# Kernel optimization log

Hardware: AMD Instinct MI355X
Metric: run time of the kernel (lower is better)

Reference implementation:

```python
import jax, jax.numpy as jnp
import numpy as np


def apply_rope(x):
    # x: [B, T, H, D]
    T, D = x.shape[1], x.shape[3]
    inv_freq = 1.0 / (10000.0 ** (jnp.arange(0, D, 2, dtype=jnp.float32) / D))  # [D/2]
    t = jnp.arange(T, dtype=jnp.float32)
    freqs = jnp.outer(t, inv_freq)  # [T, D/2]
    sin_f = jnp.sin(freqs)[None, :, None, :]
    cos_f = jnp.cos(freqs)[None, :, None, :]
    x1, x2 = jnp.split(x, 2, axis=-1)
    return jnp.concatenate([x1 * cos_f - x2 * sin_f, x1 * sin_f + x2 * cos_f], axis=-1)


def setup_inputs() -> dict:
    key = jax.random.key(0)
    ks = jax.random.split(key, 5)
    B, T, D = 8, 8192, 128
    s = 1.0 / np.sqrt(D)
    return {
        "x": jax.random.normal(ks[0], (B, T, D), dtype=jnp.float32),
        "Wq": jax.random.normal(ks[1], (D, D), dtype=jnp.float32) * s,
        "bq": jnp.zeros((D,), dtype=jnp.float32),
        "Wk": jax.random.normal(ks[2], (D, D), dtype=jnp.float32) * s,
        "bk": jnp.zeros((D,), dtype=jnp.float32),
        "Wv": jax.random.normal(ks[3], (D, D), dtype=jnp.float32) * s,
        "bv": jnp.zeros((D,), dtype=jnp.float32),
        "Wo": jax.random.normal(ks[4], (D, D), dtype=jnp.float32) * s,
        "bo": jnp.zeros((D,), dtype=jnp.float32),
    }


def reference(x, Wq, bq, Wk, bk, Wv, bv, Wo, bo):
    n_heads = 8
    B, T, d_model = x.shape
    head_dim = d_model // n_heads

    q = (x @ Wq + bq).reshape(B, T, n_heads, head_dim)
    k = (x @ Wk + bk).reshape(B, T, n_heads, head_dim)
    v = (x @ Wv + bv).reshape(B, T, n_heads, head_dim)

    q = jax.nn.elu(apply_rope(q)) + 1.0
    k = jax.nn.elu(apply_rope(k)) + 1.0

    # non-causal linear attention: context = sum_t k_t v_t^T per head
    context = jnp.einsum("bthd,bthe->bhde", k, v)            # [B,H,Dh,Dh]
    out = jnp.einsum("bthd,bhde->bthe", q, context)           # [B,T,H,Dh]
    k_sum = jnp.sum(k, axis=1)                                  # [B,H,Dh]
    z = 1.0 / (jnp.einsum("bthd,bhd->bth", q, k_sum) + 1e-6)  # [B,T,H]
    out = out * z[..., None]

    out = out.reshape(B, T, d_model)
    return out @ Wo + bo
```

## Files before the change

kernel.cpp:

```cpp
#include <hip/hip_runtime.h>
#include <hip/hip_bf16.h>


typedef __attribute__((ext_vector_type(8))) short short8;
typedef __attribute__((ext_vector_type(4))) float floatx4;

#define DEV __device__ __forceinline__
#define MFMA __builtin_amdgcn_mfma_f32_16x16x32_bf16

DEV unsigned short bfh(float f) {
  unsigned int x = __float_as_uint(f);
  x += 0x7fffu + ((x >> 16) & 1u);
  return (unsigned short)(x >> 16);
}
DEV float bfdec(unsigned short u) { return __uint_as_float(((unsigned int)u) << 16); }
DEV void splitf(float f, unsigned short& h, unsigned short& l) {
  h = bfh(f);
  l = bfh(f - bfdec(h));
}
DEV void split8(const float* p, short8& h8, short8& l8) {
  float4 a = *(const float4*)p;
  float4 b = *(const float4*)(p + 4);
  float v[8] = {a.x, a.y, a.z, a.w, b.x, b.y, b.z, b.w};
  union { short8 s; unsigned short u[8]; } H, L;
#pragma unroll
  for (int i = 0; i < 8; ++i) splitf(v[i], H.u[i], L.u[i]);
  h8 = H.s; l8 = L.s;
}

DEV void xpose_frag(floatx4 m0, floatx4 m1, int lane16, int quad,
                    short8& hi, short8& lo) {
  union { short8 s; unsigned short u[8]; } H, L;
#pragma unroll
  for (int j = 0; j < 8; ++j) {
    int srcLane = lane16 + (((quad & 1) * 2 + (j >> 2)) << 4);
    float vA = __shfl(m0[j & 3], srcLane, 64);
    float vB = __shfl(m1[j & 3], srcLane, 64);
    float v = (quad < 2) ? vA : vB;
    splitf(v, H.u[j], L.u[j]);
  }
  hi = H.s; lo = L.s;
}

__global__ void k_prep(const float* __restrict__ Wq, const float* __restrict__ Wk,
                       const float* __restrict__ Wv,
                       unsigned short* __restrict__ WTh, unsigned short* __restrict__ WTl,
                       float* __restrict__ ctxz) {
  int gid = blockIdx.x * 256 + threadIdx.x;
  if (gid < 6144) {
    int mat = gid >> 11, r = gid & 2047, n = r >> 4, k0 = (r & 15) * 8;
    const float* W = (mat == 0) ? Wq : (mat == 1) ? Wk : Wv;
    union { uint4 q; unsigned short u[8]; } oh, ol;
#pragma unroll
    for (int i = 0; i < 8; ++i) splitf(W[(size_t)(k0 + i) * 128 + n], oh.u[i], ol.u[i]);
    *(uint4*)&WTh[mat * 16384 + n * 128 + k0] = oh.q;
    *(uint4*)&WTl[mat * 16384 + n * 128 + k0] = ol.q;
  } else if (gid < 6144 + 17408) {
    ctxz[gid - 6144] = 0.0f;
  }
}

__global__ __launch_bounds__(512) void k_qkv(
    const float* __restrict__ x,
    const unsigned short* __restrict__ WTh, const unsigned short* __restrict__ WTl,
    const float* __restrict__ bq, const float* __restrict__ bk, const float* __restrict__ bv,
    float* __restrict__ ctx, float* __restrict__ ksum,
    unsigned short* __restrict__ qws) {
  __shared__ unsigned short xh[64 * 136], xl[64 * 136];
  __shared__ float rc[64][9], rs[64][9];
  const int tid = threadIdx.x;
  const int row0 = blockIdx.x * 64;
  const int b = row0 >> 13;
  const int t0 = row0 & 8191;

  {
    int r = tid >> 3, j = tid & 7;
    float invf = 1.0f / powf(10000.0f, (float)j * 0.125f);
    float s, c;
    sincosf((float)(t0 + r) * invf, &s, &c);
    rc[r][j] = c; rs[r][j] = s;
  }
  {
    int r = tid >> 3, cg = (tid & 7) * 16;
    const float* xp = x + (size_t)(row0 + r) * 128 + cg;
    short8 h0, l0, h1, l1;
    split8(xp, h0, l0);
    split8(xp + 8, h1, l1);
    *(short8*)&xh[r * 136 + cg] = h0;
    *(short8*)&xh[r * 136 + cg + 8] = h1;
    *(short8*)&xl[r * 136 + cg] = l0;
    *(short8*)&xl[r * 136 + cg + 8] = l1;
  }
  __syncthreads();

  const int l = tid & 63, w = tid >> 6;
  const int lane16 = l & 15, quad = l >> 4;

  floatx4 acc[3][4];
#pragma unroll
  for (int i = 0; i < 3; ++i)
#pragma unroll
    for (int j = 0; j < 4; ++j) acc[i][j] = (floatx4){0.f, 0.f, 0.f, 0.f};

#pragma unroll
  for (int ks = 0; ks < 4; ++ks) {
    short8 afh[4], afl[4];
#pragma unroll
    for (int mt = 0; mt < 4; ++mt) {
      int off = (mt * 16 + lane16) * 136 + ks * 32 + quad * 8;
      afh[mt] = *(const short8*)&xh[off];
      afl[mt] = *(const short8*)&xl[off];
    }
#pragma unroll
    for (int mat = 0; mat < 3; ++mat) {
      size_t woff = (size_t)mat * 16384 +
                    (size_t)(w * 16 + lane16) * 128 + ks * 32 + quad * 8;
      short8 bh = *(const short8*)(WTh + woff);
      short8 bl = *(const short8*)(WTl + woff);
#pragma unroll
      for (int mt = 0; mt < 4; ++mt) {
        acc[mat][mt] = MFMA(afh[mt], bh, acc[mat][mt], 0, 0, 0);
        acc[mat][mt] = MFMA(afl[mt], bh, acc[mat][mt], 0, 0, 0);
        acc[mat][mt] = MFMA(afh[mt], bl, acc[mat][mt], 0, 0, 0);
      }
    }
  }

  {
    int col = w * 16 + lane16;
    float bias[3] = {bq[col], bk[col], bv[col]};
#pragma unroll
    for (int mat = 0; mat < 3; ++mat)
#pragma unroll
      for (int mt = 0; mt < 4; ++mt)
#pragma unroll
        for (int r = 0; r < 4; ++r) acc[mat][mt][r] += bias[mat];
  }

  {
    const int d = lane16, j = d & 7;
#pragma unroll
    for (int mt = 0; mt < 4; ++mt) {
      float cc[4], ss[4];
#pragma unroll
      for (int r = 0; r < 4; ++r) {
        int tl = mt * 16 + quad * 4 + r;
        cc[r] = rc[tl][j]; ss[r] = rs[tl][j];
      }
#pragma unroll
      for (int mat = 0; mat < 2; ++mat) {
#pragma unroll
        for (int r = 0; r < 4; ++r) {
          float v = acc[mat][mt][r];
          float p = __shfl_xor(v, 8);
          float nv = (d < 8) ? (v * cc[r] - p * ss[r]) : (p * ss[r] + v * cc[r]);
          acc[mat][mt][r] = (nv > 0.f) ? (nv + 1.f) : __expf(nv);
        }
      }
    }
  }

  {
    float s = 0.f;
#pragma unroll
    for (int mt = 0; mt < 4; ++mt)
#pragma unroll
      for (int r = 0; r < 4; ++r) s += acc[1][mt][r];
    s += __shfl_xor(s, 16);
    s += __shfl_xor(s, 32);
    if (l < 16) atomicAdd(&ksum[(b * 8 + w) * 16 + lane16], s);
  }

#pragma unroll
  for (int mt = 0; mt < 4; ++mt)
#pragma unroll
    for (int r = 0; r < 4; ++r)
      qws[(size_t)(row0 + mt * 16 + quad * 4 + r) * 128 + w * 16 + lane16] =
          bfh(acc[0][mt][r]);

  {
    floatx4 c = (floatx4){0.f, 0.f, 0.f, 0.f};
#pragma unroll
    for (int ks2 = 0; ks2 < 2; ++ks2) {
      short8 kh, kl, vh, vl;
      xpose_frag(acc[1][ks2 * 2], acc[1][ks2 * 2 + 1], lane16, quad, kh, kl);
      xpose_frag(acc[2][ks2 * 2], acc[2][ks2 * 2 + 1], lane16, quad, vh, vl);
      c = MFMA(kh, vh, c, 0, 0, 0);
      c = MFMA(kl, vh, c, 0, 0, 0);
      c = MFMA(kh, vl, c, 0, 0, 0);
    }
#pragma unroll
    for (int r = 0; r < 4; ++r)
      atomicAdd(&ctx[((size_t)(b * 8 + w) * 16 + quad * 4 + r) * 16 + lane16], c[r]);
  }
}

__global__ void k_mprep(const float* __restrict__ Wo, const float* __restrict__ ctx,
                        unsigned short* __restrict__ MTh, unsigned short* __restrict__ MTl) {
  int gid = blockIdx.x * 256 + threadIdx.x;
  int b = gid >> 11, r = gid & 2047, oc = r >> 4, qcg = r & 15;
  int h = qcg >> 1, d0 = (qcg & 1) * 8;
  const float* C = ctx + (size_t)(b * 8 + h) * 256;
  float m[8] = {0.f, 0.f, 0.f, 0.f, 0.f, 0.f, 0.f, 0.f};
#pragma unroll 4
  for (int e = 0; e < 16; ++e) {
    float wv = Wo[(size_t)(h * 16 + e) * 128 + oc];
#pragma unroll
    for (int i = 0; i < 8; ++i) m[i] += C[(d0 + i) * 16 + e] * wv;
  }
  union { uint4 q; unsigned short u[8]; } oh, ol;
#pragma unroll
  for (int i = 0; i < 8; ++i) splitf(m[i], oh.u[i], ol.u[i]);
  *(uint4*)&MTh[(size_t)gid * 8] = oh.q;
  *(uint4*)&MTl[(size_t)gid * 8] = ol.q;
}

__global__ __launch_bounds__(256) void k_zout(
    const unsigned short* __restrict__ qws,
    const unsigned short* __restrict__ MTh, const unsigned short* __restrict__ MTl,
    const float* __restrict__ bo, const float* __restrict__ ksum,
    float* __restrict__ out) {
  __shared__ float ksumS[128], boS[128];
  const int tid = threadIdx.x;
  const int row0 = blockIdx.x * 128;
  const int b = row0 >> 13;

  if (tid < 128) ksumS[tid] = ksum[b * 128 + tid];
  else boS[tid - 128] = bo[tid - 128];
  __syncthreads();

  const int l = tid & 63, w = tid >> 6;
  const int lane16 = l & 15, quad = l >> 4;
  const unsigned short* MThb = MTh + (size_t)b * 16384;
  const unsigned short* MTlb = MTl + (size_t)b * 16384;

  short8 ah[2][4], al[2][4];
#pragma unroll
  for (int mt2 = 0; mt2 < 2; ++mt2) {
    int trow = row0 + w * 32 + mt2 * 16 + lane16;
#pragma unroll
    for (int ks = 0; ks < 4; ++ks) {
      union { short8 s8; unsigned short u[8]; } qq;
      qq.s8 = *(const short8*)&qws[(size_t)trow * 128 + ks * 32 + quad * 8];
      int kb = ks * 32 + quad * 8;
      float s = 0.f;
#pragma unroll
      for (int j = 0; j < 8; ++j) s += bfdec(qq.u[j]) * ksumS[kb + j];
      s += __shfl_xor(s, 16);
      float z = 1.0f / (s + 1e-6f);
      union { short8 s8; unsigned short u[8]; } H, L;
#pragma unroll
      for (int j = 0; j < 8; ++j) splitf(bfdec(qq.u[j]) * z, H.u[j], L.u[j]);
      ah[mt2][ks] = H.s8;
      al[mt2][ks] = L.s8;
    }
  }

  floatx4 oacc[2][8];
#pragma unroll
  for (int i = 0; i < 2; ++i)
#pragma unroll
    for (int j = 0; j < 8; ++j) oacc[i][j] = (floatx4){0.f, 0.f, 0.f, 0.f};

#pragma unroll
  for (int nt = 0; nt < 8; ++nt) {
#pragma unroll
    for (int ks = 0; ks < 4; ++ks) {
      size_t off = (size_t)(nt * 16 + lane16) * 128 + ks * 32 + quad * 8;
      short8 wbh = *(const short8*)(MThb + off);
      short8 wbl = *(const short8*)(MTlb + off);
#pragma unroll
      for (int mt2 = 0; mt2 < 2; ++mt2) {
        oacc[mt2][nt] = MFMA(ah[mt2][ks], wbh, oacc[mt2][nt], 0, 0, 0);
        oacc[mt2][nt] = MFMA(al[mt2][ks], wbh, oacc[mt2][nt], 0, 0, 0);
        oacc[mt2][nt] = MFMA(ah[mt2][ks], wbl, oacc[mt2][nt], 0, 0, 0);
      }
    }
  }

#pragma unroll
  for (int nt = 0; nt < 8; ++nt) {
    int oc = nt * 16 + lane16;
    float bb = boS[oc];
#pragma unroll
    for (int mt2 = 0; mt2 < 2; ++mt2)
#pragma unroll
      for (int r = 0; r < 4; ++r) {
        int t = row0 + w * 32 + mt2 * 16 + quad * 4 + r;
        out[(size_t)t * 128 + oc] = oacc[mt2][nt][r] + bb;
      }
  }
}

extern "C" void kernel_launch(void* const* d_in, const int* in_sizes, int n_in,
                              void* d_out, int out_size, void* d_ws, size_t ws_size,
                              hipStream_t stream) {
  const float* x  = (const float*)d_in[0];
  const float* Wq = (const float*)d_in[1];
  const float* bq = (const float*)d_in[2];
  const float* Wk = (const float*)d_in[3];
  const float* bk = (const float*)d_in[4];
  const float* Wv = (const float*)d_in[5];
  const float* bv = (const float*)d_in[6];
  const float* Wo = (const float*)d_in[7];
  const float* bo = (const float*)d_in[8];
  float* out = (float*)d_out;

  unsigned short* qws = (unsigned short*)d_ws;
  unsigned short* WTh = qws + 8388608;
  unsigned short* WTl = WTh + 49152;
  float* ctx  = (float*)(WTl + 49152);
  float* ksum = ctx + 16384;
  unsigned short* MTh = (unsigned short*)(ksum + 1024);
  unsigned short* MTl = MTh + 131072;

  k_prep<<<92, 256, 0, stream>>>(Wq, Wk, Wv, WTh, WTl, ctx);
  k_qkv<<<1024, 512, 0, stream>>>(x, WTh, WTl, bq, bk, bv, ctx, ksum, qws);
  k_mprep<<<64, 256, 0, stream>>>(Wo, ctx, MTh, MTl);
  k_zout<<<512, 256, 0, stream>>>(qws, MTh, MTl, bo, ksum, out);
}
```

Before: 171.6 us.

## Stage output weights in LDS via async loads and double-buffer QKV weight fragments

In the projection kernel, each wave now loads its weight fragments for the next k-step before running the current step's MFMAs, so global load latency overlaps with compute. k_mprep writes the fused context·Wo matrix in an MFMA-fragment-ordered layout. k_zout copies that per-batch matrix into 64 KB of LDS with asynchronous global-to-LDS loads issued before the z computation, then reads contiguous LDS fragments instead of strided global reads. The 64 KB of shared memory per block reduces occupancy and adds a one-time copy per block.

```diff
diff --git a/kernel.cpp b/kernel.cpp
--- a/kernel.cpp
+++ b/kernel.cpp
@@ -40,6 +40,12 @@
     splitf(v, H.u[j], L.u[j]);
   }
   hi = H.s; lo = L.s;
+}
+
+DEV void async16(const void* g, void* l) {
+  __builtin_amdgcn_global_load_lds(
+      (const __attribute__((address_space(1))) unsigned int*)g,
+      (__attribute__((address_space(3))) unsigned int*)l, 16, 0, 0);
 }
 
 __global__ void k_prep(const float* __restrict__ Wq, const float* __restrict__ Wk,
@@ -102,8 +108,28 @@
 #pragma unroll
     for (int j = 0; j < 4; ++j) acc[i][j] = (floatx4){0.f, 0.f, 0.f, 0.f};
 
+  size_t wbase[3];
+#pragma unroll
+  for (int mat = 0; mat < 3; ++mat)
+    wbase[mat] = (size_t)mat * 16384 + (size_t)(w * 16 + lane16) * 128 + quad * 8;
+
+  short8 wh[2][3], wl[2][3];
+#pragma unroll
+  for (int mat = 0; mat < 3; ++mat) {
+    wh[0][mat] = *(const short8*)(WTh + wbase[mat]);
+    wl[0][mat] = *(const short8*)(WTl + wbase[mat]);
+  }
+
 #pragma unroll
   for (int ks = 0; ks < 4; ++ks) {
+    const int cur = ks & 1, nxt = cur ^ 1;
+    if (ks < 3) {
+#pragma unroll
+      for (int mat = 0; mat < 3; ++mat) {
+        wh[nxt][mat] = *(const short8*)(WTh + wbase[mat] + (ks + 1) * 32);
+        wl[nxt][mat] = *(const short8*)(WTl + wbase[mat] + (ks + 1) * 32);
+      }
+    }
     short8 afh[4], afl[4];
 #pragma unroll
     for (int mt = 0; mt < 4; ++mt) {
@@ -113,15 +139,11 @@
     }
 #pragma unroll
     for (int mat = 0; mat < 3; ++mat) {
-      size_t woff = (size_t)mat * 16384 +
-                    (size_t)(w * 16 + lane16) * 128 + ks * 32 + quad * 8;
-      short8 bh = *(const short8*)(WTh + woff);
-      short8 bl = *(const short8*)(WTl + woff);
 #pragma unroll
       for (int mt = 0; mt < 4; ++mt) {
-        acc[mat][mt] = MFMA(afh[mt], bh, acc[mat][mt], 0, 0, 0);
-        acc[mat][mt] = MFMA(afl[mt], bh, acc[mat][mt], 0, 0, 0);
-        acc[mat][mt] = MFMA(afh[mt], bl, acc[mat][mt], 0, 0, 0);
+        acc[mat][mt] = MFMA(afh[mt], wh[cur][mat], acc[mat][mt], 0, 0, 0);
+        acc[mat][mt] = MFMA(afl[mt], wh[cur][mat], acc[mat][mt], 0, 0, 0);
+        acc[mat][mt] = MFMA(afh[mt], wl[cur][mat], acc[mat][mt], 0, 0, 0);
       }
     }
   }
@@ -211,8 +233,9 @@
   union { uint4 q; unsigned short u[8]; } oh, ol;
 #pragma unroll
   for (int i = 0; i < 8; ++i) splitf(m[i], oh.u[i], ol.u[i]);
-  *(uint4*)&MTh[(size_t)gid * 8] = oh.q;
-  *(uint4*)&MTl[(size_t)gid * 8] = ol.q;
+  int grp = (((oc >> 4) * 4 + (qcg >> 2)) * 64) + (qcg & 3) * 16 + (oc & 15);
+  *(uint4*)&MTh[(size_t)b * 16384 + grp * 8] = oh.q;
+  *(uint4*)&MTl[(size_t)b * 16384 + grp * 8] = ol.q;
 }
 
 __global__ __launch_bounds__(256) void k_zout(
@@ -220,19 +243,27 @@
     const unsigned short* __restrict__ MTh, const unsigned short* __restrict__ MTl,
     const float* __restrict__ bo, const float* __restrict__ ksum,
     float* __restrict__ out) {
+  __shared__ __align__(16) unsigned short mh[16384], ml[16384];
   __shared__ float ksumS[128], boS[128];
   const int tid = threadIdx.x;
   const int row0 = blockIdx.x * 128;
   const int b = row0 >> 13;
-
+  const int l = tid & 63, w = tid >> 6;
+  const int lane16 = l & 15, quad = l >> 4;
+
+  {
+    const char* gh = (const char*)(MTh + (size_t)b * 16384);
+    const char* gl = (const char*)(MTl + (size_t)b * 16384);
+#pragma unroll
+    for (int i = 0; i < 8; ++i) {
+      int off = (i * 4 + w) * 1024 + l * 16;
+      async16(gh + off, (char*)mh + off);
+      async16(gl + off, (char*)ml + off);
+    }
+  }
   if (tid < 128) ksumS[tid] = ksum[b * 128 + tid];
   else boS[tid - 128] = bo[tid - 128];
   __syncthreads();
-
-  const int l = tid & 63, w = tid >> 6;
-  const int lane16 = l & 15, quad = l >> 4;
-  const unsigned short* MThb = MTh + (size_t)b * 16384;
-  const unsigned short* MTlb = MTl + (size_t)b * 16384;
 
   short8 ah[2][4], al[2][4];
 #pragma unroll
@@ -266,9 +297,9 @@
   for (int nt = 0; nt < 8; ++nt) {
 #pragma unroll
     for (int ks = 0; ks < 4; ++ks) {
-      size_t off = (size_t)(nt * 16 + lane16) * 128 + ks * 32 + quad * 8;
-      short8 wbh = *(const short8*)(MThb + off);
-      short8 wbl = *(const short8*)(MTlb + off);
+      int moff = ((nt * 4 + ks) * 64 + l) * 8;
+      short8 wbh = *(const short8*)&mh[moff];
+      short8 wbl = *(const short8*)&ml[moff];
 #pragma unroll
       for (int mt2 = 0; mt2 < 2; ++mt2) {
         oacc[mt2][nt] = MFMA(ah[mt2][ks], wbh, oacc[mt2][nt], 0, 0, 0);
```

Result: faster. 159.4 us (-7.1%).
